# Kernel tuning notes

Measured on AMD Instinct MI355X. Metric: run time of the kernel, lower is better.

The kernel has to match this reference:

```python
import jax, jax.numpy as jnp
import numpy as np

L, H, P = 16384, 1024, 512
DT_MIN, DT_MAX = 1e-3, 1e-1
STEP_RESCALE = 1.0


def setup_inputs() -> dict:
    key = jax.random.key(0)
    ks = jax.random.split(key, 7)
    input_sequence = jax.random.normal(ks[0], (L, H), jnp.float32)
    # eigenvalues with negative real part (left half plane), HiPPO-like imag parts
    Lambda_re = -(jax.random.uniform(ks[1], (P,), jnp.float32) * 0.9 + 0.1)
    Lambda_im = jnp.pi * jnp.arange(P, dtype=jnp.float32)
    B = jax.random.normal(ks[2], (P, H, 2), jnp.float32) / jnp.sqrt(2.0 * H)   # real/imag of B_tilde (P,H)
    C = jax.random.normal(ks[3], (H, P, 2), jnp.float32) / jnp.sqrt(2.0 * P)   # real/imag of C_tilde (H,P)
    D = jax.random.normal(ks[4], (H,), jnp.float32)
    u01 = jax.random.uniform(ks[5], (P, 1), jnp.float32)
    log_step = jnp.log(DT_MIN) + u01 * (jnp.log(DT_MAX) - jnp.log(DT_MIN))     # (P,1)
    return dict(input_sequence=input_sequence, Lambda_re=Lambda_re, Lambda_im=Lambda_im,
                B=B, C=C, D=D, log_step=log_step)


def _binop(q_i, q_j):
    # diagonal linear recurrence composition: (A, b) pairs
    A_i, b_i = q_i
    A_j, b_j = q_j
    return A_j * A_i, A_j * b_i + b_j


def reference(input_sequence, Lambda_re, Lambda_im, B, C, D, log_step):
    Lambda = Lambda_re + 1j * Lambda_im                        # (P,) complex64
    B_tilde = B[..., 0] + 1j * B[..., 1]                       # (P,H)
    C_tilde = C[..., 0] + 1j * C[..., 1]                       # (H,P)
    step = STEP_RESCALE * jnp.exp(log_step[:, 0])              # (P,)
    # ZOH discretization
    Lambda_bar = jnp.exp(Lambda * step)                        # (P,)
    B_bar = ((Lambda_bar - 1.0) / Lambda)[:, None] * B_tilde   # (P,H)
    # Bu_elements: (L,P) complex
    Bu = input_sequence.astype(B_bar.dtype) @ B_bar.T
    Lambda_elems = jnp.broadcast_to(Lambda_bar, Bu.shape)      # (L,P)
    # parallel associative scan over the diagonal recurrence x_t = Lambda_bar*x_{t-1} + Bu_t
    _, xs = jax.lax.associative_scan(_binop, (Lambda_elems, Bu))
    ys = 2.0 * (xs @ C_tilde.T).real                           # conj_sym => factor 2, (L,H)
    return ys + D * input_sequence
```

## Files before the change

kernel.cpp:

```cpp
#include <hip/hip_runtime.h>
#include <math.h>

#define L_SEQ 16384
#define H_DIM 1024
#define P_DIM 512
#define N2P   1024
#define KDIM  1024
#define NTILE 32
#define CHUNK 64
#define NCHUNK 256

typedef __attribute__((ext_vector_type(8))) short short8;
typedef __attribute__((ext_vector_type(4))) float f32x4;
typedef __attribute__((address_space(3))) const char* lds3_t;

__device__ __forceinline__ unsigned short f2bf(float f){
    unsigned int u = __float_as_uint(f);
    u = (u + 0x7FFFu + ((u >> 16) & 1u)) >> 16;
    return (unsigned short)u;
}
__device__ __forceinline__ float bf2f(unsigned int lo16){
    return __uint_as_float(lo16 << 16);
}

__global__ void k_prep_lambda(const float* __restrict__ lre, const float* __restrict__ lim,
                              const float* __restrict__ lstep,
                              float* __restrict__ lam, float* __restrict__ coef,
                              float* __restrict__ lpow)
{
    int p = threadIdx.x;
    double step = exp((double)lstep[p]);
    double dr = (double)lre[p], di = (double)lim[p];
    double ar = dr*step, ai = di*step;
    double er = exp(ar);
    double lbr = er*cos(ai), lbi = er*sin(ai);
    lam[2*p] = (float)lbr; lam[2*p+1] = (float)lbi;
    double nr = lbr - 1.0, ni = lbi;
    double d2 = dr*dr + di*di;
    coef[2*p]   = (float)((nr*dr + ni*di)/d2);
    coef[2*p+1] = (float)((ni*dr - nr*di)/d2);
    double xr = lbr, xi = lbi;
    #pragma unroll
    for (int s=0;s<6;s++){ double t = xr*xr - xi*xi; xi = 2.0*xr*xi; xr = t; }
    lpow[2*p] = (float)xr; lpow[2*p+1] = (float)xi;
}

__global__ __launch_bounds__(256)
void k_prep_BB(const float* __restrict__ B, const float* __restrict__ coef,
               unsigned short* __restrict__ BB)
{
    int i = blockIdx.x*256 + threadIdx.x;
    int p = i >> 10, h = i & 1023;
    float br = B[2*i], bi = B[2*i+1];
    float cr = coef[2*p], ci = coef[2*p+1];
    BB[(size_t)(2*p)*H_DIM + h]   = f2bf(cr*br - ci*bi);
    BB[(size_t)(2*p+1)*H_DIM + h] = f2bf(cr*bi + ci*br);
}

__global__ __launch_bounds__(256)
void k_prep_CC(const float* __restrict__ C, unsigned short* __restrict__ CC)
{
    int i = blockIdx.x*256 + threadIdx.x;
    int h = i >> 9, p = i & 511;
    float cr = C[2*i], ci = C[2*i+1];
    CC[(size_t)h*N2P + 2*p]     = f2bf(2.f*cr);
    CC[(size_t)h*N2P + 2*p + 1] = f2bf(-2.f*ci);
}

__global__ __launch_bounds__(256)
void k_cast(const float4* __restrict__ u, unsigned short* __restrict__ o)
{
    int i = blockIdx.x*256 + threadIdx.x;
    float4 a = u[2*i], b = u[2*i+1];
    union { short8 v; unsigned short s[8]; } r;
    r.s[0]=f2bf(a.x); r.s[1]=f2bf(a.y); r.s[2]=f2bf(a.z); r.s[3]=f2bf(a.w);
    r.s[4]=f2bf(b.x); r.s[5]=f2bf(b.y); r.s[6]=f2bf(b.z); r.s[7]=f2bf(b.w);
    *reinterpret_cast<short8*>(o + (size_t)i*8) = r.v;
}

template<int EPI>
__global__ __launch_bounds__(512, 2)
void gemm256(const unsigned short* __restrict__ A, const unsigned short* __restrict__ Bm,
             float* __restrict__ Cf, unsigned short* __restrict__ Cb,
             const float* __restrict__ Dv, const unsigned short* __restrict__ U16)
{
    __shared__ char lds[131072];
    const int tid  = threadIdx.x;
    const int lane = tid & 63;
    const int wid  = tid >> 6;
    const int wm = wid >> 2, wn = wid & 3;
    const int wg = ((int)blockIdx.x & 7) * 32 + ((int)blockIdx.x >> 3);
    const int tm = wg >> 2, tn = wg & 3;
    const int lr = lane & 15;

    const int srow = wid*16 + (lane >> 2);
    const int scol = (((lane & 3) ^ ((lane >> 3) & 3)) << 3);
    const size_t aS0 = (size_t)(tm*256 + srow) * KDIM + scol;
    const size_t bS0 = (size_t)(tn*256 + srow) * KDIM + scol;
    const int ldsW = wid * 1024;

    const int kc   = (((lane >> 4) ^ ((lr >> 1) & 3)) << 4);
    const int aOff = (wm*128 + lr)*64 + kc;
    const int bOff = (wn*64  + lr)*64 + kc;

#define GLOAD(SRC, DST) __builtin_amdgcn_global_load_lds( \
        (const __attribute__((address_space(1))) void*)(SRC), \
        (__attribute__((address_space(3))) void*)(DST), 16, 0, 0)
#define STAGE_A(tt) do{ int bb_ = ((tt)&3)*16384; \
    const unsigned short* s_ = A + aS0 + (size_t)(tt)*32; \
    GLOAD(s_,                    lds + bb_ + ldsW); \
    GLOAD(s_ + (size_t)128*KDIM, lds + bb_ + 8192 + ldsW); }while(0)
#define STAGE_B(tt) do{ int bb_ = 65536 + ((tt)&3)*16384; \
    const unsigned short* s_ = Bm + bS0 + (size_t)(tt)*32; \
    GLOAD(s_,                    lds + bb_ + ldsW); \
    GLOAD(s_ + (size_t)128*KDIM, lds + bb_ + 8192 + ldsW); }while(0)
#define DSR(D, P, IMM) asm volatile("ds_read_b128 %0, %1 offset:" IMM : "=v"(D) : "v"(P))
#define MFMA(a,b,c) __builtin_amdgcn_mfma_f32_16x16x32_bf16(a,b,c,0,0,0)
#define BAR __builtin_amdgcn_s_barrier()

    short8 af[8], bfr[4];
    f32x4 acc[8][4];
    #pragma unroll
    for (int m=0;m<8;m++)
        #pragma unroll
        for (int n=0;n<4;n++) acc[m][n] = (f32x4){0.f,0.f,0.f,0.f};

    STAGE_A(0); STAGE_B(0); STAGE_A(1); STAGE_B(1); STAGE_A(2); STAGE_B(2);

    for (int t = 0; t < NTILE; ++t) {
        const int sb = (t & 3) * 16384;
        const int tt = (t < NTILE-3) ? t+3 : NTILE-1;
        STAGE_A(tt);
        STAGE_B(tt);
        asm volatile("s_waitcnt vmcnt(12)" ::: "memory");
        BAR;
        lds3_t pa = (lds3_t)(lds + sb + aOff);
        lds3_t pb = (lds3_t)(lds + 65536 + sb + bOff);
        DSR(af[0], pa, "0");    DSR(af[1], pa, "1024");
        DSR(af[2], pa, "2048"); DSR(af[3], pa, "3072");
        DSR(af[4], pa, "4096"); DSR(af[5], pa, "5120");
        DSR(af[6], pa, "6144"); DSR(af[7], pa, "7168");
        DSR(bfr[0], pb, "0");    DSR(bfr[1], pb, "1024");
        DSR(bfr[2], pb, "2048"); DSR(bfr[3], pb, "3072");
        asm volatile("s_waitcnt lgkmcnt(0)" ::: "memory");
        __builtin_amdgcn_sched_barrier(0);
        __builtin_amdgcn_s_setprio(1);
        #pragma unroll
        for (int m=0;m<8;m++){
            acc[m][0] = MFMA(af[m], bfr[0], acc[m][0]);
            acc[m][1] = MFMA(af[m], bfr[1], acc[m][1]);
            acc[m][2] = MFMA(af[m], bfr[2], acc[m][2]);
            acc[m][3] = MFMA(af[m], bfr[3], acc[m][3]);
        }
        __builtin_amdgcn_s_setprio(0);
        BAR;
    }
    asm volatile("s_waitcnt vmcnt(0)" ::: "memory");

    const int orow0 = tm*256 + wm*128 + (lane>>4)*4;
    const int ocol0 = tn*256 + wn*64 + lr;
    #pragma unroll
    for (int m=0;m<8;m++){
        #pragma unroll
        for (int n=0;n<4;n++){
            int row = orow0 + m*16, col = ocol0 + n*16;
            #pragma unroll
            for (int j=0;j<4;j++){
                size_t idx = (size_t)(row + j)*N2P + col;
                if (EPI) Cf[idx] = acc[m][n][j] + Dv[col]*bf2f(U16[idx]);
                else     Cb[idx] = f2bf(acc[m][n][j]);
            }
        }
    }
#undef GLOAD
#undef STAGE_A
#undef STAGE_B
#undef DSR
#undef MFMA
#undef BAR
}

__global__ __launch_bounds__(512)
void k_agg(const unsigned int* __restrict__ Bu, const float* __restrict__ lam,
           float* __restrict__ agg)
{
    int p = threadIdx.x, c = blockIdx.x;
    float lrr = lam[2*p], lii = lam[2*p+1];
    float xr = 0.f, xi = 0.f;
    const unsigned int* b2 = Bu + (size_t)c*CHUNK*512 + p;
    #pragma unroll 4
    for (int t=0;t<CHUNK;t++){
        unsigned int b = b2[(size_t)t*512];
        float br = __uint_as_float(b << 16);
        float bi = __uint_as_float(b & 0xffff0000u);
        float tr = lrr*xr - lii*xi + br;
        xi = lrr*xi + lii*xr + bi;
        xr = tr;
    }
    agg[((size_t)c*P_DIM + p)*2]     = xr;
    agg[((size_t)c*P_DIM + p)*2 + 1] = xi;
}

__global__ __launch_bounds__(256)
void k_scan(const float* __restrict__ agg, const float* __restrict__ lpow,
            float* __restrict__ xinit)
{
    __shared__ float sr[NCHUNK], si[NCHUNK];
    int c = threadIdx.x, p = blockIdx.x;
    float xr = agg[((size_t)c*P_DIM + p)*2];
    float xi = agg[((size_t)c*P_DIM + p)*2 + 1];
    sr[c] = xr; si[c] = xi;
    float wr = lpow[2*p], wi = lpow[2*p+1];
    for (int s=1; s<NCHUNK; s<<=1){
        __syncthreads();
        float ur = 0.f, ui = 0.f;
        if (c >= s){ ur = sr[c-s]; ui = si[c-s]; }
        __syncthreads();
        xr += wr*ur - wi*ui;
        xi += wr*ui + wi*ur;
        sr[c] = xr; si[c] = xi;
        float t = wr*wr - wi*wi; wi = 2.f*wr*wi; wr = t;
    }
    __syncthreads();
    float er = 0.f, ei = 0.f;
    if (c > 0){ er = sr[c-1]; ei = si[c-1]; }
    xinit[((size_t)c*P_DIM + p)*2]     = er;
    xinit[((size_t)c*P_DIM + p)*2 + 1] = ei;
}

__global__ __launch_bounds__(512)
void k_apply(const unsigned int* __restrict__ Bu, const float* __restrict__ lam,
             const float* __restrict__ xinit, unsigned int* __restrict__ xs)
{
    int p = threadIdx.x, c = blockIdx.x;
    float lrr = lam[2*p], lii = lam[2*p+1];
    float xr = xinit[((size_t)c*P_DIM + p)*2];
    float xi = xinit[((size_t)c*P_DIM + p)*2 + 1];
    const unsigned int* b2 = Bu + (size_t)c*CHUNK*512 + p;
    unsigned int* o = xs + (size_t)c*CHUNK*512 + p;
    #pragma unroll 4
    for (int t=0;t<CHUNK;t++){
        unsigned int b = b2[(size_t)t*512];
        float br = __uint_as_float(b << 16);
        float bi = __uint_as_float(b & 0xffff0000u);
        float tr = lrr*xr - lii*xi + br;
        xi = lrr*xi + lii*xr + bi;
        xr = tr;
        o[(size_t)t*512] = (unsigned int)f2bf(xr) | ((unsigned int)f2bf(xi) << 16);
    }
}

extern "C" void kernel_launch(void* const* d_in, const int* in_sizes, int n_in,
                              void* d_out, int out_size, void* d_ws, size_t ws_size,
                              hipStream_t stream)
{
    const float* u   = (const float*)d_in[0];
    const float* lre = (const float*)d_in[1];
    const float* lim = (const float*)d_in[2];
    const float* B   = (const float*)d_in[3];
    const float* C   = (const float*)d_in[4];
    const float* D   = (const float*)d_in[5];
    const float* ls  = (const float*)d_in[6];
    float* out = (float*)d_out;

    char* w = (char*)d_ws;
    unsigned short* u16  = (unsigned short*)(w + 0);
    unsigned short* xs16 = (unsigned short*)(w + 33554432);
    unsigned short* Bu16 = (unsigned short*)(w + 67108864);
    unsigned short* BB   = (unsigned short*)(w + 100663296);
    unsigned short* CC   = (unsigned short*)(w + 102760448);
    float* lam   = (float*)(w + 104857600);
    float* coef  = (float*)(w + 104861696);
    float* lpow  = (float*)(w + 104865792);
    float* agg   = (float*)(w + 104869888);
    float* xinit = (float*)(w + 105918464);

    k_prep_lambda<<<1, P_DIM, 0, stream>>>(lre, lim, ls, lam, coef, lpow);
    k_prep_BB<<<(P_DIM*H_DIM)/256, 256, 0, stream>>>(B, coef, BB);
    k_prep_CC<<<(H_DIM*P_DIM)/256, 256, 0, stream>>>(C, CC);
    k_cast<<<(L_SEQ*H_DIM)/(256*8), 256, 0, stream>>>((const float4*)u, u16);

    gemm256<0><<<256, 512, 0, stream>>>(u16, BB, nullptr, Bu16, nullptr, nullptr);

    k_agg<<<NCHUNK, P_DIM, 0, stream>>>((const unsigned int*)Bu16, lam, agg);
    k_scan<<<P_DIM, NCHUNK, 0, stream>>>(agg, lpow, xinit);
    k_apply<<<NCHUNK, P_DIM, 0, stream>>>((const unsigned int*)Bu16, lam, xinit,
                                          (unsigned int*)xs16);

    gemm256<1><<<256, 512, 0, stream>>>(xs16, CC, out, nullptr, D, u16);
}
```

Baseline: 136.8 us.

## Restructure GEMM main loop into K=64 double-buffered tiles with interleaved phases

The bf16 GEMM main loop now uses 64-wide K tiles in a two-slot LDS double buffer instead of 32-wide tiles in a four-slot ring. Each K tile is split into four MFMA phases, with the LDS fragment reads and the next A/B global-to-LDS loads interleaved between phases, and the A and B loads staggered by different prefetch distances. A wider XOR swizzle is used to avoid LDS bank conflicts. The goal is finer-grained overlap of memory traffic with MFMA work and fewer loop iterations. The cost is more barriers per tile and tricky buffer-reuse timing that could race or stall.

```diff
diff --git a/kernel.cpp b/kernel.cpp
--- a/kernel.cpp
+++ b/kernel.cpp
@@ -6,7 +6,7 @@
 #define P_DIM 512
 #define N2P   1024
 #define KDIM  1024
-#define NTILE 32
+#define NKT   16
 #define CHUNK 64
 #define NCHUNK 256
 
@@ -93,67 +93,95 @@
     const int tm = wg >> 2, tn = wg & 3;
     const int lr = lane & 15;
 
-    const int srow = wid*16 + (lane >> 2);
-    const int scol = (((lane & 3) ^ ((lane >> 3) & 3)) << 3);
-    const size_t aS0 = (size_t)(tm*256 + srow) * KDIM + scol;
-    const size_t bS0 = (size_t)(tn*256 + srow) * KDIM + scol;
-    const int ldsW = wid * 1024;
-
-    const int kc   = (((lane >> 4) ^ ((lr >> 1) & 3)) << 4);
-    const int aOff = (wm*128 + lr)*64 + kc;
-    const int bOff = (wn*64  + lr)*64 + kc;
+    const int scol = ((tid & 7) ^ ((tid >> 3) & 7)) << 3;
+    const int srow = tid >> 3;
+    const int kc0 = (((lane >> 4)      ^ (lr & 7)) << 4);
+    const int kc1 = ((((lane >> 4) | 4) ^ (lr & 7)) << 4);
+    const int aSub = wm*16384 + lr*128;
+    const int bSub = 32768 + (wn >> 1)*16384 + (wn & 1)*8192 + lr*128;
 
 #define GLOAD(SRC, DST) __builtin_amdgcn_global_load_lds( \
         (const __attribute__((address_space(1))) void*)(SRC), \
         (__attribute__((address_space(3))) void*)(DST), 16, 0, 0)
-#define STAGE_A(tt) do{ int bb_ = ((tt)&3)*16384; \
-    const unsigned short* s_ = A + aS0 + (size_t)(tt)*32; \
-    GLOAD(s_,                    lds + bb_ + ldsW); \
-    GLOAD(s_ + (size_t)128*KDIM, lds + bb_ + 8192 + ldsW); }while(0)
-#define STAGE_B(tt) do{ int bb_ = 65536 + ((tt)&3)*16384; \
-    const unsigned short* s_ = Bm + bS0 + (size_t)(tt)*32; \
-    GLOAD(s_,                    lds + bb_ + ldsW); \
-    GLOAD(s_ + (size_t)128*KDIM, lds + bb_ + 8192 + ldsW); }while(0)
+#define STAGE_A(kt_, h_) do{ \
+    char* d_ = lds + (((kt_)&1)<<16) + (h_)*16384 + tid*16; \
+    const unsigned short* s_ = A + (size_t)(tm*256 + (h_)*128 + srow)*KDIM + (size_t)(kt_)*64 + scol; \
+    GLOAD(s_, d_); GLOAD(s_ + (size_t)64*KDIM, d_ + 8192); }while(0)
+#define STAGE_B(kt_, h_) do{ \
+    char* d_ = lds + (((kt_)&1)<<16) + 32768 + (h_)*16384 + tid*16; \
+    const unsigned short* s_ = Bm + (size_t)(tn*256 + (h_)*128 + srow)*KDIM + (size_t)(kt_)*64 + scol; \
+    GLOAD(s_, d_); GLOAD(s_ + (size_t)64*KDIM, d_ + 8192); }while(0)
 #define DSR(D, P, IMM) asm volatile("ds_read_b128 %0, %1 offset:" IMM : "=v"(D) : "v"(P))
+#define LGKM0 do{ asm volatile("s_waitcnt lgkmcnt(0)" ::: "memory"); \
+                  __builtin_amdgcn_sched_barrier(0); }while(0)
+#define VMC4  asm volatile("s_waitcnt vmcnt(4)" ::: "memory")
 #define MFMA(a,b,c) __builtin_amdgcn_mfma_f32_16x16x32_bf16(a,b,c,0,0,0)
 #define BAR __builtin_amdgcn_s_barrier()
-
-    short8 af[8], bfr[4];
+#define PRIO1 __builtin_amdgcn_s_setprio(1)
+#define PRIO0 __builtin_amdgcn_s_setprio(0)
+
+    short8 a1[4], a2[4], bb0[4], bb1[4];
     f32x4 acc[8][4];
     #pragma unroll
     for (int m=0;m<8;m++)
         #pragma unroll
         for (int n=0;n<4;n++) acc[m][n] = (f32x4){0.f,0.f,0.f,0.f};
 
-    STAGE_A(0); STAGE_B(0); STAGE_A(1); STAGE_B(1); STAGE_A(2); STAGE_B(2);
-
-    for (int t = 0; t < NTILE; ++t) {
-        const int sb = (t & 3) * 16384;
-        const int tt = (t < NTILE-3) ? t+3 : NTILE-1;
-        STAGE_A(tt);
-        STAGE_B(tt);
-        asm volatile("s_waitcnt vmcnt(12)" ::: "memory");
-        BAR;
-        lds3_t pa = (lds3_t)(lds + sb + aOff);
-        lds3_t pb = (lds3_t)(lds + 65536 + sb + bOff);
-        DSR(af[0], pa, "0");    DSR(af[1], pa, "1024");
-        DSR(af[2], pa, "2048"); DSR(af[3], pa, "3072");
-        DSR(af[4], pa, "4096"); DSR(af[5], pa, "5120");
-        DSR(af[6], pa, "6144"); DSR(af[7], pa, "7168");
-        DSR(bfr[0], pb, "0");    DSR(bfr[1], pb, "1024");
-        DSR(bfr[2], pb, "2048"); DSR(bfr[3], pb, "3072");
-        asm volatile("s_waitcnt lgkmcnt(0)" ::: "memory");
-        __builtin_amdgcn_sched_barrier(0);
-        __builtin_amdgcn_s_setprio(1);
-        #pragma unroll
-        for (int m=0;m<8;m++){
-            acc[m][0] = MFMA(af[m], bfr[0], acc[m][0]);
-            acc[m][1] = MFMA(af[m], bfr[1], acc[m][1]);
-            acc[m][2] = MFMA(af[m], bfr[2], acc[m][2]);
-            acc[m][3] = MFMA(af[m], bfr[3], acc[m][3]);
-        }
-        __builtin_amdgcn_s_setprio(0);
-        BAR;
+    STAGE_A(0,0); STAGE_A(0,1); STAGE_B(0,0); STAGE_B(0,1); STAGE_B(1,0); STAGE_B(1,1);
+    VMC4; BAR;
+
+    for (int kt = 0; kt < NKT; ++kt) {
+        const int sb = (kt & 1) << 16;
+        const int tA = (kt+1 < NKT) ? kt+1 : NKT-1;
+        const int tB = (kt+2 < NKT) ? kt+2 : NKT-1;
+        lds3_t pa0 = (lds3_t)(lds + sb + aSub + kc0);
+        lds3_t pa1 = (lds3_t)(lds + sb + aSub + kc1);
+        lds3_t pb0 = (lds3_t)(lds + sb + bSub + kc0);
+        lds3_t pb1 = (lds3_t)(lds + sb + bSub + kc1);
+
+        DSR(a1[0], pa0, "0");    DSR(a1[1], pa0, "2048");
+        DSR(a1[2], pa0, "4096"); DSR(a1[3], pa0, "6144");
+        DSR(bb0[0], pb0, "0");    DSR(bb0[1], pb0, "2048");
+        DSR(bb0[2], pb0, "4096"); DSR(bb0[3], pb0, "6144");
+        STAGE_A(tA, 0);
+        BAR; LGKM0; PRIO1;
+        #pragma unroll
+        for (int m=0;m<4;m++)
+            #pragma unroll
+            for (int n=0;n<4;n++) acc[m][n] = MFMA(a1[m], bb0[n], acc[m][n]);
+        PRIO0; BAR;
+
+        DSR(a2[0], pa0, "8192");  DSR(a2[1], pa0, "10240");
+        DSR(a2[2], pa0, "12288"); DSR(a2[3], pa0, "14336");
+        STAGE_A(tA, 1);
+        BAR; LGKM0; PRIO1;
+        #pragma unroll
+        for (int m=0;m<4;m++)
+            #pragma unroll
+            for (int n=0;n<4;n++) acc[4+m][n] = MFMA(a2[m], bb0[n], acc[4+m][n]);
+        PRIO0; BAR;
+
+        DSR(a1[0], pa1, "0");    DSR(a1[1], pa1, "2048");
+        DSR(a1[2], pa1, "4096"); DSR(a1[3], pa1, "6144");
+        DSR(bb1[0], pb1, "0");    DSR(bb1[1], pb1, "2048");
+        DSR(bb1[2], pb1, "4096"); DSR(bb1[3], pb1, "6144");
+        BAR; LGKM0; PRIO1;
+        #pragma unroll
+        for (int m=0;m<4;m++)
+            #pragma unroll
+            for (int n=0;n<4;n++) acc[m][n] = MFMA(a1[m], bb1[n], acc[m][n]);
+        PRIO0; BAR;
+
+        DSR(a2[0], pa1, "8192");  DSR(a2[1], pa1, "10240");
+        DSR(a2[2], pa1, "12288"); DSR(a2[3], pa1, "14336");
+        STAGE_B(tB, 0); STAGE_B(tB, 1);
+        VMC4;
+        BAR; LGKM0; PRIO1;
+        #pragma unroll
+        for (int m=0;m<4;m++)
+            #pragma unroll
+            for (int n=0;n<4;n++) acc[4+m][n] = MFMA(a2[m], bb1[n], acc[4+m][n]);
+        PRIO0; BAR;
     }
     asm volatile("s_waitcnt vmcnt(0)" ::: "memory");
 
@@ -176,8 +204,12 @@
 #undef STAGE_A
 #undef STAGE_B
 #undef DSR
+#undef LGKM0
+#undef VMC4
 #undef MFMA
 #undef BAR
+#undef PRIO1
+#undef PRIO0
 }
 
 __global__ __launch_bounds__(512)
```

Measured after the change: 134.6 us. No clear change (-1.6%).
